# Performance work log

Hardware: AMD Instinct MI355X
Metric: run time of the kernel (lower is better)

The kernel has to match this reference:

```python
import jax, jax.numpy as jnp
import numpy as np

RPN_SCALES = (2.0, 4.0, 8.0, 16.0)   # feature-map strides per pyramid level
BASE_SIZES = (8.0, 16.0, 32.0, 64.0) # rpn_base_sizes: nearest-size level assignment
CROP_SIZE = 14                        # output crop resolution
IMG = 512


def setup_inputs() -> dict:
    key = jax.random.key(0)
    kf0, kf1, kf2, kf3, kx, ky, ks, ka, ksc = jax.random.split(key, 9)
    C = 256
    f0 = jax.random.normal(kf0, (1, C, 256, 256), dtype=jnp.float32)
    f1 = jax.random.normal(kf1, (1, C, 128, 128), dtype=jnp.float32)
    f2 = jax.random.normal(kf2, (1, C, 64, 64), dtype=jnp.float32)
    f3 = jax.random.normal(kf3, (1, C, 32, 32), dtype=jnp.float32)

    N = 1024
    # box sizes log-uniform in [4, 128] so every pyramid level is exercised
    s = 2.0 ** jax.random.uniform(ks, (N,), minval=2.0, maxval=7.0)
    ar = jax.random.uniform(ka, (N,), minval=0.7, maxval=1.4)
    w = s * jnp.sqrt(ar)
    h = s / jnp.sqrt(ar)
    x0 = jax.random.uniform(kx, (N,), minval=0.0, maxval=IMG - 1.0 - 128.0)
    y0 = jax.random.uniform(ky, (N,), minval=0.0, maxval=IMG - 1.0 - 128.0)
    x1 = jnp.minimum(x0 + w, IMG - 1.0)
    y1 = jnp.minimum(y0 + h, IMG - 1.0)
    score = jax.random.uniform(ksc, (N,))
    bidx = jnp.zeros((N,), dtype=jnp.float32)  # single image in batch
    proposals = jnp.stack([bidx, x0, y0, x1, y1, score, jnp.zeros((N,))], axis=1).astype(jnp.float32)
    return {"f0": f0, "f1": f1, "f2": f2, "f3": f3, "proposals": proposals}


def _roi_crop(f, rois, stride):
    """ROIAlign-style bilinear crop. f: [B,C,H,W], rois: [N,5] (b,x0,y0,x1,y1 image coords).
    Returns [N, C, S, S]."""
    S = CROP_SIZE
    H, W = f.shape[2], f.shape[3]
    b = rois[:, 0].astype(jnp.int32)
    x0, y0, x1, y1 = (rois[:, i] / stride for i in (1, 2, 3, 4))
    bw = (x1 - x0) / S
    bh = (y1 - y0) / S
    grid = jnp.arange(S, dtype=f.dtype) + 0.5
    xs = x0[:, None] + grid[None, :] * bw[:, None] - 0.5   # [N,S] sample centers
    ys = y0[:, None] + grid[None, :] * bh[:, None] - 0.5

    def split(coord, M):
        c0 = jnp.floor(coord)
        frac = coord - c0
        i0 = jnp.clip(c0.astype(jnp.int32), 0, M - 1)
        i1 = jnp.clip(i0 + 1, 0, M - 1)
        return i0, i1, frac

    yi0, yi1, wy = split(ys, H)
    xi0, xi1, wx = split(xs, W)
    bb = b[:, None, None]                                   # [N,1,1]

    def g(yi, xi):
        # advanced indexing with middle slice -> [N,S,S,C]
        return f[bb, :, yi[:, :, None], xi[:, None, :]]

    wy = wy[:, :, None, None]                               # [N,S,1,1]
    wx = wx[:, None, :, None]                               # [N,1,S,1]
    v = (g(yi0, xi0) * (1 - wy) * (1 - wx)
         + g(yi0, xi1) * (1 - wy) * wx
         + g(yi1, xi0) * wy * (1 - wx)
         + g(yi1, xi1) * wy * wx)                            # [N,S,S,C]
    return jnp.transpose(v, (0, 3, 1, 2))                   # [N,C,S,S]


def reference(f0, f1, f2, f3, proposals):
    boxes = proposals[:, 1:5]
    sizes = jnp.sqrt((boxes[:, 2] - boxes[:, 0]) * (boxes[:, 3] - boxes[:, 1]))
    dist = jnp.abs(sizes[:, None] - jnp.asarray(BASE_SIZES, dtype=sizes.dtype)[None, :])
    min_index = jnp.argmin(dist, axis=1)                    # per-proposal level assignment
    rois = proposals[:, 0:5]
    # route -> compute -> combine, expressed as compute-all-levels + per-proposal select
    # (identical math to gather-per-level + sort-restore in the original)
    crops_all = jnp.stack([_roi_crop(f, rois, s)
                           for f, s in zip((f0, f1, f2, f3), RPN_SCALES)])  # [L,N,C,S,S]
    return crops_all[min_index, jnp.arange(rois.shape[0])]  # [N,C,S,S]
```

## Files before the change

### kernel.cpp

```cpp
#include <hip/hip_runtime.h>

#define CROP_S 14
#define NPIX   196
#define NCH    256
#define CPB    16
#define NGRP   (NCH / CPB)
#define PROWS  12
#define PCOLS  16
#define PSZ    (PROWS * PCOLS)
#define STAGE_V4 (CPB * PSZ / 4)

__global__ __launch_bounds__(256) void roi_crop_kernel(
    const float* __restrict__ f0, const float* __restrict__ f1,
    const float* __restrict__ f2, const float* __restrict__ f3,
    const float* __restrict__ proposals, float* __restrict__ out)
{
    __shared__ float s_patch[CPB * PSZ];

    const int bid = blockIdx.x;
    const int n   = bid >> 4;
    const int cg  = bid & (NGRP - 1);
    const int c0  = cg * CPB;
    const int tid = threadIdx.x;

    const float px0 = proposals[n * 7 + 1];
    const float py0 = proposals[n * 7 + 2];
    const float px1 = proposals[n * 7 + 3];
    const float py1 = proposals[n * 7 + 4];

    const float size = sqrtf((px1 - px0) * (py1 - py0));
    int lvl = 0;
    float bd = fabsf(size - 8.0f);
    {
        float d1 = fabsf(size - 16.0f);
        if (d1 < bd) { bd = d1; lvl = 1; }
        float d2 = fabsf(size - 32.0f);
        if (d2 < bd) { bd = d2; lvl = 2; }
        float d3 = fabsf(size - 64.0f);
        if (d3 < bd) { bd = d3; lvl = 3; }
    }

    const float* f = (lvl == 0) ? f0 : (lvl == 1) ? f1 : (lvl == 2) ? f2 : f3;
    const float stride = (float)(2 << lvl);
    const int   M      = 256 >> lvl;
    const int   HW     = M * M;

    const float x0s = px0 / stride, y0s = py0 / stride;
    const float x1s = px1 / stride, y1s = py1 / stride;
    const float bw = (x1s - x0s) / (float)CROP_S;
    const float bh = (y1s - y0s) / (float)CROP_S;

    const int ylo  = min(max((int)floorf(y0s + 0.5f * bh - 0.5f), 0), M - 1);
    int xlo4 = min(max((int)floorf(x0s + 0.5f * bw - 0.5f), 0), M - 1) & ~3;
    xlo4 = min(xlo4, M - PCOLS);

    {
        const float* fbase = f + (size_t)c0 * HW + xlo4;
        #pragma unroll
        for (int it = 0; it < STAGE_V4 / 256; ++it) {
            const int sidx = it * 256 + tid;
            const int c    = sidx / (PSZ / 4);
            const int rem  = sidx - c * (PSZ / 4);
            const int r    = rem >> 2;
            const int q    = rem & 3;
            const int gy   = min(ylo + r, M - 1);
            const float4 v = *reinterpret_cast<const float4*>(
                fbase + (size_t)c * HW + gy * M + q * 4);
            *reinterpret_cast<float4*>(&s_patch[sidx * 4]) = v;
        }
    }
    __syncthreads();

    if (tid >= NPIX) return;

    const int y = tid / CROP_S;
    const int x = tid - y * CROP_S;
    const float xs = x0s + ((float)x + 0.5f) * bw - 0.5f;
    const float ys = y0s + ((float)y + 0.5f) * bh - 0.5f;
    const float fx = floorf(xs), fy = floorf(ys);
    const float wx = xs - fx;
    const float wy = ys - fy;
    const int xi0 = min(max((int)fx, 0), M - 1);
    const int yi0 = min(max((int)fy, 0), M - 1);
    const int ci0 = min(xi0 - xlo4, PCOLS - 2);
    const int ri0 = min(yi0 - ylo,  PROWS - 2);
    const int o00 = ri0 * PCOLS + ci0;

    float* op = out + (size_t)n * NCH * NPIX + (size_t)c0 * NPIX + tid;

    #pragma unroll
    for (int c = 0; c < CPB; ++c) {
        const float* pp = s_patch + c * PSZ + o00;
        const float v00 = pp[0];
        const float v10 = pp[PCOLS];
        const float v01 = pp[1];
        const float v11 = pp[PCOLS + 1];
        const float r0 = v00 + wx * (v01 - v00);
        const float r1 = v10 + wx * (v11 - v10);
        const float v  = r0 + wy * (r1 - r0);
        op[0] = v;
        op += NPIX;
    }
}

extern "C" void kernel_launch(void* const* d_in, const int* in_sizes, int n_in,
                              void* d_out, int out_size, void* d_ws, size_t ws_size,
                              hipStream_t stream) {
    const float* f0 = (const float*)d_in[0];
    const float* f1 = (const float*)d_in[1];
    const float* f2 = (const float*)d_in[2];
    const float* f3 = (const float*)d_in[3];
    const float* proposals = (const float*)d_in[4];
    float* out = (float*)d_out;

    const int N = in_sizes[4] / 7;

    roi_crop_kernel<<<dim3(N * NGRP), dim3(256), 0, stream>>>(f0, f1, f2, f3, proposals, out);
}
```

Baseline: 67.73 us.

## Make blocks persistent over several items and prefetch the next patch into registers

Each block now handles up to 8 (proposal, channel-group) items in a grid-stride loop. While it interpolates the current item from shared memory, it issues the global loads for the next item's patch into registers and prefetches the proposal coordinates two items ahead. Output writes become nontemporal stores, and the level scale uses a multiply instead of a divide. This aims to hide global load latency within a block, at the cost of fewer blocks, more registers per thread and two barriers per item.

New measurement: 133.1 us. 1.96x slower.

```diff
diff --git a/kernel.cpp b/kernel.cpp
--- a/kernel.cpp
+++ b/kernel.cpp
@@ -8,98 +8,133 @@
 #define PROWS  12
 #define PCOLS  16
 #define PSZ    (PROWS * PCOLS)
-#define STAGE_V4 (CPB * PSZ / 4)
+#define ITEMS  8
+
+struct Ctx {
+    const float* fbase;
+    int   M, HW, ylo;
+    float wx, wy;
+    int   o00;
+    float* op;
+};
 
 __global__ __launch_bounds__(256) void roi_crop_kernel(
     const float* __restrict__ f0, const float* __restrict__ f1,
     const float* __restrict__ f2, const float* __restrict__ f3,
-    const float* __restrict__ proposals, float* __restrict__ out)
+    const float* __restrict__ proposals, float* __restrict__ out,
+    int n_items)
 {
     __shared__ float s_patch[CPB * PSZ];
+    const int tid = threadIdx.x;
+    const int b   = blockIdx.x;
+    const int strideb = gridDim.x;
 
-    const int bid = blockIdx.x;
-    const int n   = bid >> 4;
-    const int cg  = bid & (NGRP - 1);
-    const int c0  = cg * CPB;
-    const int tid = threadIdx.x;
+    auto make_ctx = [&](float px0, float py0, float px1, float py1,
+                        int item, Ctx& ic) {
+        const float size = sqrtf((px1 - px0) * (py1 - py0));
+        int lvl = 0; float bd = fabsf(size - 8.f), d;
+        d = fabsf(size - 16.f); if (d < bd) { bd = d; lvl = 1; }
+        d = fabsf(size - 32.f); if (d < bd) { bd = d; lvl = 2; }
+        d = fabsf(size - 64.f); if (d < bd) { bd = d; lvl = 3; }
+        const float* f = (lvl==0)?f0:(lvl==1)?f1:(lvl==2)?f2:f3;
+        const float inv = (lvl==0)?0.5f:(lvl==1)?0.25f:(lvl==2)?0.125f:0.0625f;
+        const int M = 256 >> lvl;
+        ic.M = M; ic.HW = M * M;
+        const float x0s = px0*inv, y0s = py0*inv, x1s = px1*inv, y1s = py1*inv;
+        const float bw = (x1s - x0s) * (1.f/CROP_S);
+        const float bh = (y1s - y0s) * (1.f/CROP_S);
+        ic.ylo = min(max((int)floorf(y0s + 0.5f*bh - 0.5f), 0), M-1);
+        int xlo4 = (min(max((int)floorf(x0s + 0.5f*bw - 0.5f), 0), M-1)) & ~3;
+        xlo4 = min(xlo4, M - PCOLS);
+        const int n  = item >> 4;
+        const int c0 = (item & 15) * CPB;
+        ic.fbase = f + (size_t)c0 * ic.HW + xlo4;
+        const int y = tid / CROP_S;
+        const int x = tid - y * CROP_S;
+        const float xs = x0s + ((float)x + 0.5f)*bw - 0.5f;
+        const float ys = y0s + ((float)y + 0.5f)*bh - 0.5f;
+        const float fx = floorf(xs), fy = floorf(ys);
+        ic.wx = xs - fx; ic.wy = ys - fy;
+        const int xi0 = min(max((int)fx, 0), M-1);
+        const int yi0 = min(max((int)fy, 0), M-1);
+        const int ci0 = min(max(xi0 - xlo4, 0), PCOLS-2);
+        const int ri0 = min(max(yi0 - ic.ylo, 0), PROWS-2);
+        ic.o00 = ri0 * PCOLS + ci0;
+        ic.op  = out + (size_t)n * (NCH*NPIX) + (size_t)c0 * NPIX + tid;
+    };
 
-    const float px0 = proposals[n * 7 + 1];
-    const float py0 = proposals[n * 7 + 2];
-    const float px1 = proposals[n * 7 + 3];
-    const float py1 = proposals[n * 7 + 4];
+    auto issue = [&](const Ctx& ic, float4& v0, float4& v1, float4& v2) {
+        const float* fb = ic.fbase;
+        const int M = ic.M, HW = ic.HW, ylo = ic.ylo;
+        {   const int sidx = tid;
+            const int c = sidx / 48, rem = sidx - c*48;
+            const int gy = min(ylo + (rem>>2), M-1);
+            v0 = *reinterpret_cast<const float4*>(fb + (size_t)c*HW + gy*M + (rem&3)*4); }
+        {   const int sidx = 256 + tid;
+            const int c = sidx / 48, rem = sidx - c*48;
+            const int gy = min(ylo + (rem>>2), M-1);
+            v1 = *reinterpret_cast<const float4*>(fb + (size_t)c*HW + gy*M + (rem&3)*4); }
+        {   const int sidx = 512 + tid;
+            const int c = sidx / 48, rem = sidx - c*48;
+            const int gy = min(ylo + (rem>>2), M-1);
+            v2 = *reinterpret_cast<const float4*>(fb + (size_t)c*HW + gy*M + (rem&3)*4); }
+    };
 
-    const float size = sqrtf((px1 - px0) * (py1 - py0));
-    int lvl = 0;
-    float bd = fabsf(size - 8.0f);
-    {
-        float d1 = fabsf(size - 16.0f);
-        if (d1 < bd) { bd = d1; lvl = 1; }
-        float d2 = fabsf(size - 32.0f);
-        if (d2 < bd) { bd = d2; lvl = 2; }
-        float d3 = fabsf(size - 64.0f);
-        if (d3 < bd) { bd = d3; lvl = 3; }
-    }
+    auto stage_write = [&](const float4& v0, const float4& v1, const float4& v2) {
+        *reinterpret_cast<float4*>(&s_patch[(size_t)tid*4])       = v0;
+        *reinterpret_cast<float4*>(&s_patch[(size_t)(256+tid)*4]) = v1;
+        *reinterpret_cast<float4*>(&s_patch[(size_t)(512+tid)*4]) = v2;
+    };
 
-    const float* f = (lvl == 0) ? f0 : (lvl == 1) ? f1 : (lvl == 2) ? f2 : f3;
-    const float stride = (float)(2 << lvl);
-    const int   M      = 256 >> lvl;
-    const int   HW     = M * M;
+    auto interp = [&](const Ctx& ic) {
+        if (tid < NPIX) {
+            const float wx = ic.wx, wy = ic.wy;
+            float* op = ic.op;
+            #pragma unroll
+            for (int c = 0; c < CPB; ++c) {
+                const float* pp = s_patch + c*PSZ + ic.o00;
+                const float v00 = pp[0], v10 = pp[PCOLS];
+                const float v01 = pp[1], v11 = pp[PCOLS+1];
+                const float r0 = v00 + wx*(v01 - v00);
+                const float r1 = v10 + wx*(v11 - v10);
+                __builtin_nontemporal_store(r0 + wy*(r1 - r0), op + c*NPIX);
+            }
+        }
+    };
 
-    const float x0s = px0 / stride, y0s = py0 / stride;
-    const float x1s = px1 / stride, y1s = py1 / stride;
-    const float bw = (x1s - x0s) / (float)CROP_S;
-    const float bh = (y1s - y0s) / (float)CROP_S;
+    Ctx    ic[2];
+    float4 sv[2][3];
+    float  pr[2][4];
 
-    const int ylo  = min(max((int)floorf(y0s + 0.5f * bh - 0.5f), 0), M - 1);
-    int xlo4 = min(max((int)floorf(x0s + 0.5f * bw - 0.5f), 0), M - 1) & ~3;
-    xlo4 = min(xlo4, M - PCOLS);
-
-    {
-        const float* fbase = f + (size_t)c0 * HW + xlo4;
-        #pragma unroll
-        for (int it = 0; it < STAGE_V4 / 256; ++it) {
-            const int sidx = it * 256 + tid;
-            const int c    = sidx / (PSZ / 4);
-            const int rem  = sidx - c * (PSZ / 4);
-            const int r    = rem >> 2;
-            const int q    = rem & 3;
-            const int gy   = min(ylo + r, M - 1);
-            const float4 v = *reinterpret_cast<const float4*>(
-                fbase + (size_t)c * HW + gy * M + q * 4);
-            *reinterpret_cast<float4*>(&s_patch[sidx * 4]) = v;
-        }
-    }
-    __syncthreads();
-
-    if (tid >= NPIX) return;
-
-    const int y = tid / CROP_S;
-    const int x = tid - y * CROP_S;
-    const float xs = x0s + ((float)x + 0.5f) * bw - 0.5f;
-    const float ys = y0s + ((float)y + 0.5f) * bh - 0.5f;
-    const float fx = floorf(xs), fy = floorf(ys);
-    const float wx = xs - fx;
-    const float wy = ys - fy;
-    const int xi0 = min(max((int)fx, 0), M - 1);
-    const int yi0 = min(max((int)fy, 0), M - 1);
-    const int ci0 = min(xi0 - xlo4, PCOLS - 2);
-    const int ri0 = min(yi0 - ylo,  PROWS - 2);
-    const int o00 = ri0 * PCOLS + ci0;
-
-    float* op = out + (size_t)n * NCH * NPIX + (size_t)c0 * NPIX + tid;
+    {   const int n0 = b >> 4;
+        pr[0][0] = proposals[n0*7+1]; pr[0][1] = proposals[n0*7+2];
+        pr[0][2] = proposals[n0*7+3]; pr[0][3] = proposals[n0*7+4]; }
+    make_ctx(pr[0][0],pr[0][1],pr[0][2],pr[0][3], b, ic[0]);
+    issue(ic[0], sv[0][0], sv[0][1], sv[0][2]);
+    {   const int item1 = b + strideb;
+        if (item1 < n_items) {
+            const int n1 = item1 >> 4;
+            pr[1][0] = proposals[n1*7+1]; pr[1][1] = proposals[n1*7+2];
+            pr[1][2] = proposals[n1*7+3]; pr[1][3] = proposals[n1*7+4]; } }
 
     #pragma unroll
-    for (int c = 0; c < CPB; ++c) {
-        const float* pp = s_patch + c * PSZ + o00;
-        const float v00 = pp[0];
-        const float v10 = pp[PCOLS];
-        const float v01 = pp[1];
-        const float v11 = pp[PCOLS + 1];
-        const float r0 = v00 + wx * (v01 - v00);
-        const float r1 = v10 + wx * (v11 - v10);
-        const float v  = r0 + wy * (r1 - r0);
-        op[0] = v;
-        op += NPIX;
+    for (int k = 0; k < ITEMS; ++k) {
+        const int cur = k & 1, nxt = cur ^ 1;
+        if (b + k*strideb >= n_items) break;
+        stage_write(sv[cur][0], sv[cur][1], sv[cur][2]);
+        __syncthreads();
+        if (k < ITEMS-1 && b + (k+1)*strideb < n_items) {
+            make_ctx(pr[nxt][0],pr[nxt][1],pr[nxt][2],pr[nxt][3],
+                     b + (k+1)*strideb, ic[nxt]);
+            issue(ic[nxt], sv[nxt][0], sv[nxt][1], sv[nxt][2]);
+            if (k < ITEMS-2 && b + (k+2)*strideb < n_items) {
+                const int n2 = (b + (k+2)*strideb) >> 4;
+                pr[cur][0] = proposals[n2*7+1]; pr[cur][1] = proposals[n2*7+2];
+                pr[cur][2] = proposals[n2*7+3]; pr[cur][3] = proposals[n2*7+4];
+            }
+        }
+        interp(ic[cur]);
+        __syncthreads();
     }
 }
 
@@ -114,6 +149,9 @@
     float* out = (float*)d_out;
 
     const int N = in_sizes[4] / 7;
+    const int n_items = N * NGRP;
+    const int grid = (n_items + ITEMS - 1) / ITEMS;
 
-    roi_crop_kernel<<<dim3(N * NGRP), dim3(256), 0, stream>>>(f0, f1, f2, f3, proposals, out);
+    roi_crop_kernel<<<dim3(grid), dim3(256), 0, stream>>>(
+        f0, f1, f2, f3, proposals, out, n_items);
 }
```
